# Kernel optimization log

Hardware: AMD Instinct MI355X
Metric: run time of the kernel (lower is better)

## Reference

```python
import jax, jax.numpy as jnp
import numpy as np

DIM = 512
BATCH, SEQ = 4, 4096


def setup_inputs() -> dict:
    key = jax.random.key(0)
    kx, kq, kk, kv, ko = jax.random.split(key, 5)
    s = DIM ** -0.5  # fan-in style init scale for stability
    return {
        "x": jax.random.normal(kx, (BATCH, SEQ, DIM), dtype=jnp.float32),
        "Wq": jax.random.normal(kq, (DIM, DIM), dtype=jnp.float32) * s,
        "Wk": jax.random.normal(kk, (DIM, DIM), dtype=jnp.float32) * s,
        "Wv": jax.random.normal(kv, (DIM, DIM), dtype=jnp.float32) * s,
        "Wo": jax.random.normal(ko, (DIM, DIM), dtype=jnp.float32) * s,
    }


def reference(x, Wq, Wk, Wv, Wo):
    # x: [B, S, D]; projections (torch Linear, no bias -> x @ W here)
    q = jnp.einsum('bsd,dk->bsk', x, Wq)  # [B,S,K]
    k = jnp.einsum('bsd,dk->bsk', x, Wk)  # [B,S,K]
    v = jnp.einsum('bsd,dv->bsv', x, Wv)  # [B,S,V]

    # sequential recurrence: M_t = M_{t-1} + v_t k_t^T ; y_t = M_t q_t
    def step(M, qkv_t):
        q_t, k_t, v_t = qkv_t  # each [B, K] / [B, V]
        M = M + v_t[:, :, None] * k_t[:, None, :]  # [B, V, K]
        y_t = jnp.einsum('bvk,bk->bv', M, q_t)
        return M, y_t

    M0 = jnp.zeros((x.shape[0], Wv.shape[1], Wk.shape[1]), dtype=x.dtype)
    qT = jnp.swapaxes(q, 0, 1)  # [S,B,K]
    kT = jnp.swapaxes(k, 0, 1)
    vT = jnp.swapaxes(v, 0, 1)
    _, ys = jax.lax.scan(step, M0, (qT, kT, vT))  # ys: [S,B,V]
    y = jnp.swapaxes(ys, 0, 1)  # [B,S,V]
    return jnp.einsum('bsv,vd->bsd', y, Wo)
```

## Files before the change

kernel.cpp:

```cpp
#include <hip/hip_runtime.h>
#include <hip/hip_bf16.h>

typedef __attribute__((ext_vector_type(8))) short bf16x8;
typedef __attribute__((ext_vector_type(4))) float f32x4;

__device__ inline short f2bf(float f) {
    __hip_bfloat16 h = __float2bfloat16(f);
    short s;
    __builtin_memcpy(&s, &h, 2);
    return s;
}
__device__ inline float bf2f(short s) {
    unsigned int u = ((unsigned int)(unsigned short)s) << 16;
    float f;
    __builtin_memcpy(&f, &u, 4);
    return f;
}

__device__ inline void cp16_async(const void* g, void* l) {
    __builtin_amdgcn_global_load_lds(
        (const __attribute__((address_space(1))) void*)g,
        (__attribute__((address_space(3))) void*)l, 16, 0, 0);
}


__global__ void cast_x_kernel(const float* __restrict__ x, short* __restrict__ out, int n4) {
    int i = blockIdx.x * 256 + threadIdx.x;
    if (i < n4) {
        float4 f = ((const float4*)x)[i];
        union { short s[4]; int2 v; } u;
        u.s[0] = f2bf(f.x); u.s[1] = f2bf(f.y); u.s[2] = f2bf(f.z); u.s[3] = f2bf(f.w);
        ((int2*)out)[i] = u.v;
    }
}

__global__ void transpose_cast_w(const float* __restrict__ W, short* __restrict__ WT) {
    int i = blockIdx.x * 256 + threadIdx.x;
    int n = i >> 9, k = i & 511;
    WT[i] = f2bf(W[k * 512 + n]);
}

__global__ void transpose_bf16(const short* __restrict__ in, short* __restrict__ out) {
    __shared__ short sT[64][72];
    const int t0 = blockIdx.x * 64, f0 = blockIdx.y * 64, b = blockIdx.z;
    const short* ip = in + (size_t)b * 4096 * 512;
    short* op = out + (size_t)b * 512 * 4096;
#pragma unroll
    for (int p = 0; p < 2; ++p) {
        int lin = p * 256 + threadIdx.x;
        int row = lin >> 3, col8 = (lin & 7) * 8;
        short tmp[8];
        *(int4*)tmp = *(const int4*)&ip[(size_t)(t0 + row) * 512 + f0 + col8];
#pragma unroll
        for (int s = 0; s < 8; ++s) sT[col8 + s][row] = tmp[s];
    }
    __syncthreads();
#pragma unroll
    for (int p = 0; p < 2; ++p) {
        int lin = p * 256 + threadIdx.x;
        int fr = lin >> 3, tc8 = (lin & 7) * 8;
        int4 v = *(const int4*)&sT[fr][tc8];
        *(int4*)&op[(size_t)(f0 + fr) * 4096 + t0 + tc8] = v;
    }
}


__device__ inline void mfma_tile_kloop(const short* __restrict__ A, int lda,
                                       const short* __restrict__ B, int ldb,
                                       int Kd, f32x4* acc,
                                       short* sA, short* sB) {
    const int tid = threadIdx.x;
    const int lane = tid & 63, wv = tid >> 6;
    const int quad = lane >> 4, lr = lane & 15;
    const int wr = (wv >> 1) * 64, wc = (wv & 1) * 64;
    const int c0 = tid, c1 = tid + 256;
    const int r0 = c0 >> 2, k80 = (c0 & 3) * 8;
    const int r1 = c1 >> 2, k81 = (c1 & 3) * 8;

    for (int k0 = 0; k0 < Kd; k0 += 32) {
        __syncthreads();
        cp16_async(A + (size_t)r0 * lda + k0 + k80, sA + c0 * 8);
        cp16_async(A + (size_t)r1 * lda + k0 + k81, sA + c1 * 8);
        cp16_async(B + (size_t)r0 * ldb + k0 + k80, sB + c0 * 8);
        cp16_async(B + (size_t)r1 * ldb + k0 + k81, sB + c1 * 8);
        __syncthreads();
        bf16x8 af[4], bf[4];
#pragma unroll
        for (int i = 0; i < 4; ++i)
            af[i] = *(const bf16x8*)&sA[(wr + i * 16 + lr) * 32 + quad * 8];
#pragma unroll
        for (int j = 0; j < 4; ++j)
            bf[j] = *(const bf16x8*)&sB[(wc + j * 16 + lr) * 32 + quad * 8];
#pragma unroll
        for (int i = 0; i < 4; ++i)
#pragma unroll
            for (int j = 0; j < 4; ++j)
                acc[i * 4 + j] = __builtin_amdgcn_mfma_f32_16x16x32_bf16(af[i], bf[j], acc[i * 4 + j], 0, 0, 0);
    }
}

__device__ inline void store_out(float* p, float v) { *p = v; }
__device__ inline void store_out(short* p, float v) { *p = f2bf(v); }

template <typename OutT>
__device__ inline void store_tile128(OutT* C, int ldc, const f32x4* acc) {
    const int lane = threadIdx.x & 63, wv = threadIdx.x >> 6;
    const int quad = lane >> 4, lr = lane & 15;
    const int wr = (wv >> 1) * 64, wc = (wv & 1) * 64;
#pragma unroll
    for (int i = 0; i < 4; ++i)
#pragma unroll
        for (int j = 0; j < 4; ++j)
#pragma unroll
            for (int r = 0; r < 4; ++r)
                store_out(&C[(size_t)(wr + i * 16 + quad * 4 + r) * ldc + wc + j * 16 + lr],
                          acc[i * 4 + j][r]);
}

template <typename OutT>
__global__ __launch_bounds__(256, 2) void gemm128(const short* __restrict__ A, int lda,
                                                  const short* __restrict__ B, int ldb,
                                                  OutT* __restrict__ C, int ldc, int Kd) {
    __shared__ short sA[128 * 32], sB[128 * 32];
    const short* At = A + (size_t)blockIdx.x * 128 * lda;
    const short* Bt = B + (size_t)blockIdx.y * 128 * ldb;
    OutT* Ct = C + (size_t)blockIdx.x * 128 * ldc + blockIdx.y * 128;
    f32x4 acc[16];
#pragma unroll
    for (int i = 0; i < 16; ++i) acc[i] = (f32x4){0.f, 0.f, 0.f, 0.f};
    mfma_tile_kloop(At, lda, Bt, ldb, Kd, acc, sA, sB);
    store_tile128(Ct, ldc, acc);
}


__global__ __launch_bounds__(256, 2) void phaseA(const short* __restrict__ Vt,
                                                 const short* __restrict__ Kt,
                                                 short* __restrict__ AM) {
    __shared__ short sA[128 * 32], sB[128 * 32];
    const int bc = blockIdx.z, b = bc >> 4, c = bc & 15;
    const short* Ap = Vt + ((size_t)b * 512 + blockIdx.x * 128) * 4096 + c * 256;
    const short* Bp = Kt + ((size_t)b * 512 + blockIdx.y * 128) * 4096 + c * 256;
    short* Cp = AM + (size_t)bc * 262144 + (size_t)blockIdx.x * 128 * 512 + blockIdx.y * 128;
    f32x4 acc[16];
#pragma unroll
    for (int i = 0; i < 16; ++i) acc[i] = (f32x4){0.f, 0.f, 0.f, 0.f};
    mfma_tile_kloop(Ap, 4096, Bp, 4096, 256, acc, sA, sB);
    store_tile128(Cp, 512, acc);
}

__global__ void scan_kernel(short* __restrict__ AM) {
    int i = blockIdx.x * 256 + threadIdx.x;
    int b = i >> 15;
    int vk8 = i & 32767;
    size_t base = (size_t)b * 16 * 262144 + (size_t)vk8 * 8;
    float acc[8];
#pragma unroll
    for (int s = 0; s < 8; ++s) acc[s] = 0.f;
    for (int c = 0; c < 16; ++c) {
        short* p = AM + base + (size_t)c * 262144;
        short in8[8];
        *(int4*)in8 = *(const int4*)p;
        short out8[8];
#pragma unroll
        for (int s = 0; s < 8; ++s) out8[s] = f2bf(acc[s]);
        *(int4*)p = *(const int4*)out8;
#pragma unroll
        for (int s = 0; s < 8; ++s) acc[s] += bf2f(in8[s]);
    }
}

__global__ __launch_bounds__(256, 2) void phaseS(const short* __restrict__ Q,
                                                 const short* __restrict__ K,
                                                 short* __restrict__ P) {
    __shared__ short sA[128 * 32], sB[128 * 32];
    const int bc = blockIdx.z, b = bc >> 4, c = bc & 15;
    const int mt = blockIdx.x, nt = blockIdx.y;
    short* Pt = P + (size_t)bc * 65536 + (size_t)mt * 128 * 256 + nt * 128;
    if (mt < nt) {
        const int4 z = {0, 0, 0, 0};
#pragma unroll
        for (int p = 0; p < 8; ++p) {
            int g = p * 256 + threadIdx.x;
            int row = g >> 4, c8 = (g & 15) * 8;
            *(int4*)&Pt[(size_t)row * 256 + c8] = z;
        }
        return;
    }
    const short* Ap = Q + ((size_t)(b * 4096 + c * 256 + mt * 128)) * 512;
    const short* Bp = K + ((size_t)(b * 4096 + c * 256 + nt * 128)) * 512;
    f32x4 acc[16];
#pragma unroll
    for (int i = 0; i < 16; ++i) acc[i] = (f32x4){0.f, 0.f, 0.f, 0.f};
    mfma_tile_kloop(Ap, 512, Bp, 512, 512, acc, sA, sB);
    const int lane = threadIdx.x & 63, wv = threadIdx.x >> 6;
    const int quad = lane >> 4, lr = lane & 15;
    const int wr = (wv >> 1) * 64, wc = (wv & 1) * 64;
#pragma unroll
    for (int i = 0; i < 4; ++i)
#pragma unroll
        for (int j = 0; j < 4; ++j)
#pragma unroll
            for (int r = 0; r < 4; ++r) {
                int t = mt * 128 + wr + i * 16 + quad * 4 + r;
                int jj = nt * 128 + wc + j * 16 + lr;
                float v = (jj <= t) ? acc[i * 4 + j][r] : 0.f;
                Pt[(size_t)(wr + i * 16 + quad * 4 + r) * 256 + wc + j * 16 + lr] = f2bf(v);
            }
}

__global__ __launch_bounds__(256, 2) void phaseY(const short* __restrict__ Q,
                                                 const short* __restrict__ Mpre,
                                                 const short* __restrict__ P,
                                                 const short* __restrict__ Vt,
                                                 short* __restrict__ Y) {
    __shared__ short sA[128 * 32], sB[128 * 32];
    const int bc = blockIdx.z, b = bc >> 4, c = bc & 15;
    const int mt = blockIdx.x, nt = blockIdx.y;
    f32x4 acc[16];
#pragma unroll
    for (int i = 0; i < 16; ++i) acc[i] = (f32x4){0.f, 0.f, 0.f, 0.f};
    const short* Ai = Q + ((size_t)(b * 4096 + c * 256 + mt * 128)) * 512;
    const short* Bi = Mpre + (size_t)bc * 262144 + (size_t)nt * 128 * 512;
    mfma_tile_kloop(Ai, 512, Bi, 512, 512, acc, sA, sB);
    const short* Ap = P + (size_t)bc * 65536 + (size_t)mt * 128 * 256;
    const short* Bv = Vt + ((size_t)b * 512 + nt * 128) * 4096 + c * 256;
    mfma_tile_kloop(Ap, 256, Bv, 4096, 256, acc, sA, sB);
    short* Cp = Y + ((size_t)(b * 4096 + c * 256 + mt * 128)) * 512 + nt * 128;
    store_tile128(Cp, 512, acc);
}


extern "C" void kernel_launch(void* const* d_in, const int* in_sizes, int n_in,
                              void* d_out, int out_size, void* d_ws, size_t ws_size,
                              hipStream_t stream) {
    const float* x  = (const float*)d_in[0];
    const float* Wq = (const float*)d_in[1];
    const float* Wk = (const float*)d_in[2];
    const float* Wv = (const float*)d_in[3];
    const float* Wo = (const float*)d_in[4];
    float* out = (float*)d_out;

    const size_t NTD = 16384 * 512;

    short* ws  = (short*)d_ws;
    short* Qb  = ws;
    short* Kb  = Qb + NTD;
    short* Vb  = Kb + NTD;
    short* Kt  = Vb + NTD;
    short* Vt  = Kt + NTD;
    short* P   = Vt + NTD;
    short* WqT = P + 4194304;
    short* WkT = WqT + 262144;
    short* WvT = WkT + 262144;
    short* WoT = WvT + 262144;
    short* Xb  = WoT + 262144;
    short* AM  = Xb;
    short* Yb  = Vb;

    cast_x_kernel<<<8192, 256, 0, stream>>>(x, Xb, (int)(NTD / 4));
    transpose_cast_w<<<1024, 256, 0, stream>>>(Wq, WqT);
    transpose_cast_w<<<1024, 256, 0, stream>>>(Wk, WkT);
    transpose_cast_w<<<1024, 256, 0, stream>>>(Wv, WvT);
    transpose_cast_w<<<1024, 256, 0, stream>>>(Wo, WoT);

    gemm128<short><<<dim3(128, 4), 256, 0, stream>>>(Xb, 512, WqT, 512, Qb, 512, 512);
    gemm128<short><<<dim3(128, 4), 256, 0, stream>>>(Xb, 512, WkT, 512, Kb, 512, 512);
    gemm128<short><<<dim3(128, 4), 256, 0, stream>>>(Xb, 512, WvT, 512, Vb, 512, 512);

    transpose_bf16<<<dim3(64, 8, 4), 256, 0, stream>>>(Kb, Kt);
    transpose_bf16<<<dim3(64, 8, 4), 256, 0, stream>>>(Vb, Vt);

    phaseA<<<dim3(4, 4, 64), 256, 0, stream>>>(Vt, Kt, AM);
    scan_kernel<<<512, 256, 0, stream>>>(AM);
    phaseS<<<dim3(2, 2, 64), 256, 0, stream>>>(Qb, Kb, P);
    phaseY<<<dim3(2, 4, 64), 256, 0, stream>>>(Qb, AM, P, Vt, Yb);

    gemm128<float><<<dim3(128, 4), 256, 0, stream>>>(Yb, 512, WoT, 512, out, 512, 512);
}
```

Baseline: 261.1 us.

## Fuse weight casts and QK projections, emit V transposed, deepen K-step to 64

Merges the four weight transpose-casts into one launch and the Q and K projections into one GEMM. V is computed directly in transposed layout, which removes a transpose kernel. The MFMA k-loop now stages 64 columns per barrier pair instead of 32, doubling LDS use to cut synchronisations. Causal work is trimmed: phaseS no longer zero-fills upper tiles, and phaseY limits the intra-chunk P·V loop to the lower-triangular extent. The larger LDS footprint may reduce occupancy, and the workspace layout is reshuffled.

```diff
diff --git a/kernel.cpp b/kernel.cpp
--- a/kernel.cpp
+++ b/kernel.cpp
@@ -34,10 +34,15 @@
     }
 }
 
-__global__ void transpose_cast_w(const float* __restrict__ W, short* __restrict__ WT) {
+__global__ void transpose_cast_w4(const float* __restrict__ W0, const float* __restrict__ W1,
+                                  const float* __restrict__ W2, const float* __restrict__ W3,
+                                  short* __restrict__ W4T) {
     int i = blockIdx.x * 256 + threadIdx.x;
-    int n = i >> 9, k = i & 511;
-    WT[i] = f2bf(W[k * 512 + n]);
+    int w = i >> 18;
+    int r = i & 262143;
+    int n = r >> 9, k = r & 511;
+    const float* W = (w == 0) ? W0 : (w == 1) ? W1 : (w == 2) ? W2 : W3;
+    W4T[i] = f2bf(W[k * 512 + n]);
 }
 
 __global__ void transpose_bf16(const short* __restrict__ in, short* __restrict__ out) {
@@ -65,37 +70,47 @@
 }
 
 
-__device__ inline void mfma_tile_kloop(const short* __restrict__ A, int lda,
-                                       const short* __restrict__ B, int ldb,
-                                       int Kd, f32x4* acc,
-                                       short* sA, short* sB) {
-    const int tid = threadIdx.x;
-    const int lane = tid & 63, wv = tid >> 6;
+#define LDS_DECL __shared__ short sA0[4096], sA1[4096], sB0[4096], sB1[4096]
+
+__device__ inline void mfma_kloop64(const short* __restrict__ A, int lda,
+                                    const short* __restrict__ B, int ldb,
+                                    int Kd, f32x4* acc,
+                                    short* sA0, short* sA1, short* sB0, short* sB1) {
+    const int tid = threadIdx.x, lane = tid & 63, wv = tid >> 6;
     const int quad = lane >> 4, lr = lane & 15;
     const int wr = (wv >> 1) * 64, wc = (wv & 1) * 64;
     const int c0 = tid, c1 = tid + 256;
     const int r0 = c0 >> 2, k80 = (c0 & 3) * 8;
     const int r1 = c1 >> 2, k81 = (c1 & 3) * 8;
 
-    for (int k0 = 0; k0 < Kd; k0 += 32) {
+    for (int k0 = 0; k0 < Kd; k0 += 64) {
         __syncthreads();
-        cp16_async(A + (size_t)r0 * lda + k0 + k80, sA + c0 * 8);
-        cp16_async(A + (size_t)r1 * lda + k0 + k81, sA + c1 * 8);
-        cp16_async(B + (size_t)r0 * ldb + k0 + k80, sB + c0 * 8);
-        cp16_async(B + (size_t)r1 * ldb + k0 + k81, sB + c1 * 8);
+        cp16_async(A + (size_t)r0 * lda + k0 + k80,      sA0 + c0 * 8);
+        cp16_async(A + (size_t)r1 * lda + k0 + k81,      sA0 + c1 * 8);
+        cp16_async(A + (size_t)r0 * lda + k0 + 32 + k80, sA1 + c0 * 8);
+        cp16_async(A + (size_t)r1 * lda + k0 + 32 + k81, sA1 + c1 * 8);
+        cp16_async(B + (size_t)r0 * ldb + k0 + k80,      sB0 + c0 * 8);
+        cp16_async(B + (size_t)r1 * ldb + k0 + k81,      sB0 + c1 * 8);
+        cp16_async(B + (size_t)r0 * ldb + k0 + 32 + k80, sB1 + c0 * 8);
+        cp16_async(B + (size_t)r1 * ldb + k0 + 32 + k81, sB1 + c1 * 8);
         __syncthreads();
-        bf16x8 af[4], bf[4];
-#pragma unroll
-        for (int i = 0; i < 4; ++i)
-            af[i] = *(const bf16x8*)&sA[(wr + i * 16 + lr) * 32 + quad * 8];
-#pragma unroll
-        for (int j = 0; j < 4; ++j)
-            bf[j] = *(const bf16x8*)&sB[(wc + j * 16 + lr) * 32 + quad * 8];
-#pragma unroll
-        for (int i = 0; i < 4; ++i)
+#pragma unroll
+        for (int half = 0; half < 2; ++half) {
+            const short* pa = half ? sA1 : sA0;
+            const short* pb = half ? sB1 : sB0;
+            bf16x8 af[4], bfr[4];
+#pragma unroll
+            for (int i = 0; i < 4; ++i)
+                af[i] = *(const bf16x8*)&pa[(wr + i * 16 + lr) * 32 + quad * 8];
 #pragma unroll
             for (int j = 0; j < 4; ++j)
-                acc[i * 4 + j] = __builtin_amdgcn_mfma_f32_16x16x32_bf16(af[i], bf[j], acc[i * 4 + j], 0, 0, 0);
+                bfr[j] = *(const bf16x8*)&pb[(wc + j * 16 + lr) * 32 + quad * 8];
+#pragma unroll
+            for (int i = 0; i < 4; ++i)
+#pragma unroll
+                for (int j = 0; j < 4; ++j)
+                    acc[i * 4 + j] = __builtin_amdgcn_mfma_f32_16x16x32_bf16(af[i], bfr[j], acc[i * 4 + j], 0, 0, 0);
+        }
     }
 }
 
@@ -117,18 +132,50 @@
                           acc[i * 4 + j][r]);
 }
 
+
+__global__ __launch_bounds__(256, 2) void gemm_qk(const short* __restrict__ Xb,
+                                                  const short* __restrict__ WqkT,
+                                                  short* __restrict__ Qb, short* __restrict__ Kb) {
+    LDS_DECL;
+    const short* At = Xb + (size_t)blockIdx.x * 128 * 512;
+    const short* Bt = WqkT + (size_t)blockIdx.y * 128 * 512;
+    short* Cbase = (blockIdx.y < 4) ? Qb : Kb;
+    int n0 = (blockIdx.y & 3) * 128;
+    short* Ct = Cbase + (size_t)blockIdx.x * 128 * 512 + n0;
+    f32x4 acc[16];
+#pragma unroll
+    for (int i = 0; i < 16; ++i) acc[i] = (f32x4){0.f, 0.f, 0.f, 0.f};
+    mfma_kloop64(At, 512, Bt, 512, 512, acc, sA0, sA1, sB0, sB1);
+    store_tile128(Ct, 512, acc);
+}
+
+__global__ __launch_bounds__(256, 2) void gemm_vt(const short* __restrict__ WvT,
+                                                  const short* __restrict__ Xb,
+                                                  short* __restrict__ Vt) {
+    LDS_DECL;
+    const int b = blockIdx.z;
+    const short* At = WvT + (size_t)blockIdx.x * 128 * 512;
+    const short* Bt = Xb + ((size_t)b * 4096 + blockIdx.y * 128) * 512;
+    short* Ct = Vt + (size_t)b * 512 * 4096 + (size_t)blockIdx.x * 128 * 4096 + blockIdx.y * 128;
+    f32x4 acc[16];
+#pragma unroll
+    for (int i = 0; i < 16; ++i) acc[i] = (f32x4){0.f, 0.f, 0.f, 0.f};
+    mfma_kloop64(At, 512, Bt, 512, 512, acc, sA0, sA1, sB0, sB1);
+    store_tile128(Ct, 4096, acc);
+}
+
 template <typename OutT>
 __global__ __launch_bounds__(256, 2) void gemm128(const short* __restrict__ A, int lda,
                                                   const short* __restrict__ B, int ldb,
                                                   OutT* __restrict__ C, int ldc, int Kd) {
-    __shared__ short sA[128 * 32], sB[128 * 32];
+    LDS_DECL;
     const short* At = A + (size_t)blockIdx.x * 128 * lda;
     const short* Bt = B + (size_t)blockIdx.y * 128 * ldb;
     OutT* Ct = C + (size_t)blockIdx.x * 128 * ldc + blockIdx.y * 128;
     f32x4 acc[16];
 #pragma unroll
     for (int i = 0; i < 16; ++i) acc[i] = (f32x4){0.f, 0.f, 0.f, 0.f};
-    mfma_tile_kloop(At, lda, Bt, ldb, Kd, acc, sA, sB);
+    mfma_kloop64(At, lda, Bt, ldb, Kd, acc, sA0, sA1, sB0, sB1);
     store_tile128(Ct, ldc, acc);
 }
 
@@ -136,7 +183,7 @@
 __global__ __launch_bounds__(256, 2) void phaseA(const short* __restrict__ Vt,
                                                  const short* __restrict__ Kt,
                                                  short* __restrict__ AM) {
-    __shared__ short sA[128 * 32], sB[128 * 32];
+    LDS_DECL;
     const int bc = blockIdx.z, b = bc >> 4, c = bc & 15;
     const short* Ap = Vt + ((size_t)b * 512 + blockIdx.x * 128) * 4096 + c * 256;
     const short* Bp = Kt + ((size_t)b * 512 + blockIdx.y * 128) * 4096 + c * 256;
@@ -144,7 +191,7 @@
     f32x4 acc[16];
 #pragma unroll
     for (int i = 0; i < 16; ++i) acc[i] = (f32x4){0.f, 0.f, 0.f, 0.f};
-    mfma_tile_kloop(Ap, 4096, Bp, 4096, 256, acc, sA, sB);
+    mfma_kloop64(Ap, 4096, Bp, 4096, 256, acc, sA0, sA1, sB0, sB1);
     store_tile128(Cp, 512, acc);
 }
 
@@ -172,39 +219,31 @@
 __global__ __launch_bounds__(256, 2) void phaseS(const short* __restrict__ Q,
                                                  const short* __restrict__ K,
                                                  short* __restrict__ P) {
-    __shared__ short sA[128 * 32], sB[128 * 32];
+    LDS_DECL;
     const int bc = blockIdx.z, b = bc >> 4, c = bc & 15;
     const int mt = blockIdx.x, nt = blockIdx.y;
+    if (mt < nt) return;
     short* Pt = P + (size_t)bc * 65536 + (size_t)mt * 128 * 256 + nt * 128;
-    if (mt < nt) {
-        const int4 z = {0, 0, 0, 0};
-#pragma unroll
-        for (int p = 0; p < 8; ++p) {
-            int g = p * 256 + threadIdx.x;
-            int row = g >> 4, c8 = (g & 15) * 8;
-            *(int4*)&Pt[(size_t)row * 256 + c8] = z;
-        }
-        return;
-    }
     const short* Ap = Q + ((size_t)(b * 4096 + c * 256 + mt * 128)) * 512;
     const short* Bp = K + ((size_t)(b * 4096 + c * 256 + nt * 128)) * 512;
     f32x4 acc[16];
 #pragma unroll
     for (int i = 0; i < 16; ++i) acc[i] = (f32x4){0.f, 0.f, 0.f, 0.f};
-    mfma_tile_kloop(Ap, 512, Bp, 512, 512, acc, sA, sB);
+    mfma_kloop64(Ap, 512, Bp, 512, 512, acc, sA0, sA1, sB0, sB1);
     const int lane = threadIdx.x & 63, wv = threadIdx.x >> 6;
     const int quad = lane >> 4, lr = lane & 15;
     const int wr = (wv >> 1) * 64, wc = (wv & 1) * 64;
+    const bool diag = (mt == nt);
 #pragma unroll
     for (int i = 0; i < 4; ++i)
 #pragma unroll
         for (int j = 0; j < 4; ++j)
 #pragma unroll
             for (int r = 0; r < 4; ++r) {
-                int t = mt * 128 + wr + i * 16 + quad * 4 + r;
-                int jj = nt * 128 + wc + j * 16 + lr;
-                float v = (jj <= t) ? acc[i * 4 + j][r] : 0.f;
-                Pt[(size_t)(wr + i * 16 + quad * 4 + r) * 256 + wc + j * 16 + lr] = f2bf(v);
+                int t = wr + i * 16 + quad * 4 + r;
+                int jj = wc + j * 16 + lr;
+                float v = (!diag || jj <= t) ? acc[i * 4 + j][r] : 0.f;
+                Pt[(size_t)t * 256 + jj] = f2bf(v);
             }
 }
 
@@ -213,7 +252,7 @@
                                                  const short* __restrict__ P,
                                                  const short* __restrict__ Vt,
                                                  short* __restrict__ Y) {
-    __shared__ short sA[128 * 32], sB[128 * 32];
+    LDS_DECL;
     const int bc = blockIdx.z, b = bc >> 4, c = bc & 15;
     const int mt = blockIdx.x, nt = blockIdx.y;
     f32x4 acc[16];
@@ -221,10 +260,10 @@
     for (int i = 0; i < 16; ++i) acc[i] = (f32x4){0.f, 0.f, 0.f, 0.f};
     const short* Ai = Q + ((size_t)(b * 4096 + c * 256 + mt * 128)) * 512;
     const short* Bi = Mpre + (size_t)bc * 262144 + (size_t)nt * 128 * 512;
-    mfma_tile_kloop(Ai, 512, Bi, 512, 512, acc, sA, sB);
+    mfma_kloop64(Ai, 512, Bi, 512, 512, acc, sA0, sA1, sB0, sB1);
     const short* Ap = P + (size_t)bc * 65536 + (size_t)mt * 128 * 256;
     const short* Bv = Vt + ((size_t)b * 512 + nt * 128) * 4096 + c * 256;
-    mfma_tile_kloop(Ap, 256, Bv, 4096, 256, acc, sA, sB);
+    mfma_kloop64(Ap, 256, Bv, 4096, (mt + 1) * 128, acc, sA0, sA1, sB0, sB1);
     short* Cp = Y + ((size_t)(b * 4096 + c * 256 + mt * 128)) * 512 + nt * 128;
     store_tile128(Cp, 512, acc);
 }
@@ -243,32 +282,26 @@
     const size_t NTD = 16384 * 512;
 
     short* ws  = (short*)d_ws;
-    short* Qb  = ws;
+    short* Xb  = ws;
+    short* Qb  = Xb + NTD;
     short* Kb  = Qb + NTD;
-    short* Vb  = Kb + NTD;
-    short* Kt  = Vb + NTD;
+    short* Kt  = Kb + NTD;
     short* Vt  = Kt + NTD;
     short* P   = Vt + NTD;
-    short* WqT = P + 4194304;
-    short* WkT = WqT + 262144;
-    short* WvT = WkT + 262144;
-    short* WoT = WvT + 262144;
-    short* Xb  = WoT + 262144;
-    short* AM  = Xb;
-    short* Yb  = Vb;
+    short* W4T = P + 4194304;
+    short* AM  = W4T + 1048576;
+    short* Yb  = Kb;
+
+    short* WqT = W4T;
+    short* WvT = W4T + 2 * 262144;
+    short* WoT = W4T + 3 * 262144;
 
     cast_x_kernel<<<8192, 256, 0, stream>>>(x, Xb, (int)(NTD / 4));
-    transpose_cast_w<<<1024, 256, 0, stream>>>(Wq, WqT);
-    transpose_cast_w<<<1024, 256, 0, stream>>>(Wk, WkT);
-    transpose_cast_w<<<1024, 256, 0, stream>>>(Wv, WvT);
-    transpose_cast_w<<<1024, 256, 0, stream>>>(Wo, WoT);
-
-    gemm128<short><<<dim3(128, 4), 256, 0, stream>>>(Xb, 512, WqT, 512, Qb, 512, 512);
-    gemm128<short><<<dim3(128, 4), 256, 0, stream>>>(Xb, 512, WkT, 512, Kb, 512, 512);
-    gemm128<short><<<dim3(128, 4), 256, 0, stream>>>(Xb, 512, WvT, 512, Vb, 512, 512);
-
+    transpose_cast_w4<<<4096, 256, 0, stream>>>(Wq, Wk, Wv, Wo, W4T);
+
+    gemm_qk<<<dim3(128, 8), 256, 0, stream>>>(Xb, WqT, Qb, Kb);
+    gemm_vt<<<dim3(4, 32, 4), 256, 0, stream>>>(WvT, Xb, Vt);
     transpose_bf16<<<dim3(64, 8, 4), 256, 0, stream>>>(Kb, Kt);
-    transpose_bf16<<<dim3(64, 8, 4), 256, 0, stream>>>(Vb, Vt);
 
     phaseA<<<dim3(4, 4, 64), 256, 0, stream>>>(Vt, Kt, AM);
     scan_kernel<<<512, 256, 0, stream>>>(AM);
```

Result: faster. 231.5 us (-11.3%).
